# Optimization experiments

Measured on AMD Instinct MI355X. Metric: run time of the kernel, lower is better.

The kernel has to match this reference:

```python
import jax, jax.numpy as jnp
import numpy as np

EMBED_DIM = 512
NUM_HEADS = 8
HEAD_DIM = EMBED_DIM // NUM_HEADS


def setup_inputs() -> dict:
    key = jax.random.key(0)
    k1, k2, k3, k4, k5, k6 = jax.random.split(key, 6)
    B, S, D = 2, 4096, EMBED_DIM
    scale = 1.0 / np.sqrt(D)
    return {
        "inputs": jax.random.normal(k1, (B, S, D), dtype=jnp.float32),
        "Wq": jax.random.normal(k2, (D, D), dtype=jnp.float32) * scale,
        "Wk": jax.random.normal(k3, (D, D), dtype=jnp.float32) * scale,
        "Wv": jax.random.normal(k4, (D, D), dtype=jnp.float32) * scale,
        "Wc": jax.random.normal(k5, (D, D), dtype=jnp.float32) * scale,
        "bc": jax.random.normal(k6, (D,), dtype=jnp.float32) * 0.01,
    }


def reference(inputs, Wq, Wk, Wv, Wc, bc):
    B, S, D = inputs.shape
    H, Hd = NUM_HEADS, HEAD_DIM

    def split_heads(x):
        # [B,S,D] -> [B,H,S,Hd]
        return x.reshape(B, S, H, Hd).transpose(0, 2, 1, 3)

    # nn.Linear applies x @ W.T
    q = split_heads(inputs @ Wq.T).astype(jnp.float32)
    k = split_heads(inputs @ Wk.T).astype(jnp.float32)
    v = split_heads(inputs @ Wv.T).astype(jnp.float32)

    scores = jnp.einsum("bhqd,bhkd->bhqk", q, k) / np.sqrt(Hd).astype(jnp.float32)
    weights = jax.nn.softmax(scores, axis=-1)
    attended = jnp.einsum("bhqk,bhkd->bhqd", weights, v).astype(inputs.dtype)
    attended = attended.transpose(0, 2, 1, 3).reshape(B, S, D)
    return attended @ Wc.T + bc
```

## Files before the change

### kernel.cpp

```cpp
#include <hip/hip_runtime.h>
#include <cstdint>
#include <cstddef>

typedef _Float16 half_t;
typedef half_t h8 __attribute__((ext_vector_type(8)));
typedef half_t h4 __attribute__((ext_vector_type(4)));
typedef float f4 __attribute__((ext_vector_type(4)));
typedef float f16v __attribute__((ext_vector_type(16)));
typedef unsigned int u32;

static constexpr int S_LEN  = 4096;
static constexpr int DMODEL = 512;
static constexpr int NH     = 8;
static constexpr int HD     = 64;
static constexpr int BATCH  = 2;
static constexpr int MTOK   = BATCH * S_LEN;

#define QSCALE 0.18033688011112043f

__device__ __forceinline__ void g2lds16(const void* g, void* l) {
    __builtin_amdgcn_global_load_lds(
        (const __attribute__((address_space(1))) u32*)(uintptr_t)g,
        (__attribute__((address_space(3))) u32*)(u32)(uintptr_t)l,
        16, 0, 0);
}

__device__ __forceinline__ f4 mfma16(h8 a, h8 b, f4 c) {
    return __builtin_amdgcn_mfma_f32_16x16x32_f16(a, b, c, 0, 0, 0);
}

__device__ __forceinline__ f16v mfma32(h8 a, h8 b, f16v c) {
    return __builtin_amdgcn_mfma_f32_32x32x16_f16(a, b, c, 0, 0, 0);
}

__device__ __forceinline__ u32 pkrtz(float a, float b) {
#if __has_builtin(__builtin_amdgcn_cvt_pkrtz)
    auto r = __builtin_amdgcn_cvt_pkrtz(a, b);
    return __builtin_bit_cast(u32, r);
#else
    union { half_t h[2]; u32 u; } x;
    x.h[0] = (half_t)a; x.h[1] = (half_t)b;
    return x.u;
#endif
}

__device__ __forceinline__ void plswap(u32 a, u32 b, u32& lo, u32& hi_, int hi) {
#if __has_builtin(__builtin_amdgcn_permlane32_swap)
    auto r = __builtin_amdgcn_permlane32_swap(a, b, false, false);
    lo = (u32)r[0]; hi_ = (u32)r[1];
#else
    u32 ta = __shfl_xor(a, 32);
    u32 tb = __shfl_xor(b, 32);
    lo  = hi ? tb : a;
    hi_ = hi ? b  : ta;
#endif
}

__global__ void cvt_all(const float* __restrict__ X,
                        const float* __restrict__ w0, const float* __restrict__ w1,
                        const float* __restrict__ w2, const float* __restrict__ w3,
                        half_t* __restrict__ Xh,
                        half_t* __restrict__ o0, half_t* __restrict__ o1,
                        half_t* __restrict__ o2, half_t* __restrict__ o3) {
    int bx = blockIdx.x;
    const float* in;
    half_t* out;
    float s = 1.0f;
    int i;
    if (bx < 2048) {
        in = X; out = Xh;
        i = (bx * 256 + threadIdx.x) * 8;
    } else {
        int y = (bx - 2048) >> 7;
        in  = (y==0) ? w0 : (y==1) ? w1 : (y==2) ? w2 : w3;
        out = (y==0) ? o0 : (y==1) ? o1 : (y==2) ? o2 : o3;
        if (y == 0) s = QSCALE;
        i = (((bx - 2048) & 127) * 256 + threadIdx.x) * 8;
    }
    const float4* p = (const float4*)(in + i);
    float4 a = p[0], b = p[1];
    h8 h;
    h[0]=(half_t)(a.x*s); h[1]=(half_t)(a.y*s); h[2]=(half_t)(a.z*s); h[3]=(half_t)(a.w*s);
    h[4]=(half_t)(b.x*s); h[5]=(half_t)(b.y*s); h[6]=(half_t)(b.z*s); h[7]=(half_t)(b.w*s);
    *(h8*)(out + i) = h;
}

__device__ __forceinline__ void gemm_core4(const half_t* __restrict__ A,
                                           const half_t* __restrict__ B,
                                           int m0, int n0, int Kdim,
                                           half_t* As, half_t* Bs,
                                           f4 (&acc)[4][4]) {
    const int tid  = threadIdx.x;
    const int lane = tid & 63;
    const int w    = tid >> 6;
    const int quad = lane >> 4;
    const int low  = lane & 15;
    const int wr   = (w >> 1) * 64;
    const int wc   = (w & 1) * 64;

    f4 zero = {0.f, 0.f, 0.f, 0.f};
    #pragma unroll
    for (int i = 0; i < 4; ++i)
        #pragma unroll
        for (int j = 0; j < 4; ++j) acc[i][j] = zero;

    auto stage = [&](int kk, int p) {
        #pragma unroll
        for (int it = 0; it < 2; ++it) {
            int c = tid + 256 * it;
            int row = c >> 2, cs = c & 3;
            int gc = cs ^ ((row >> 1) & 3);
            g2lds16(A + (size_t)(m0 + row) * Kdim + kk + gc * 8, As + p * 4096 + c * 8);
        }
        #pragma unroll
        for (int it = 0; it < 2; ++it) {
            int c = tid + 256 * it;
            int row = c >> 2, cs = c & 3;
            int gc = cs ^ ((row >> 1) & 3);
            g2lds16(B + (size_t)(n0 + row) * Kdim + kk + gc * 8, Bs + p * 4096 + c * 8);
        }
    };

    stage(0, 0);
    const int T = Kdim / 32;
    for (int t = 0; t < T; ++t) {
        __syncthreads();
        if (t + 1 < T) stage((t + 1) * 32, (t + 1) & 1);

        const half_t* Ac = As + (t & 1) * 4096;
        const half_t* Bc = Bs + (t & 1) * 4096;
        h8 af[4], bf[4];
        #pragma unroll
        for (int i = 0; i < 4; ++i) {
            int r = wr + i * 16 + low;
            af[i] = *(const h8*)(Ac + r * 32 + (quad ^ ((r >> 1) & 3)) * 8);
        }
        #pragma unroll
        for (int j = 0; j < 4; ++j) {
            int r = wc + j * 16 + low;
            bf[j] = *(const h8*)(Bc + r * 32 + (quad ^ ((r >> 1) & 3)) * 8);
        }
        #pragma unroll
        for (int i = 0; i < 4; ++i)
            #pragma unroll
            for (int j = 0; j < 4; ++j)
                acc[i][j] = mfma16(af[i], bf[j], acc[i][j]);
    }
}

__global__ __launch_bounds__(256, 3) void gemm_proj(
    const half_t* __restrict__ X,
    const half_t* __restrict__ Wq, const half_t* __restrict__ Wk, const half_t* __restrict__ Wv,
    half_t* __restrict__ Q, half_t* __restrict__ K, half_t* __restrict__ Vt) {
    __shared__ half_t SM[16384];
    const int z  = blockIdx.z;
    const int bx = blockIdx.x;

    const half_t *A, *B;
    int m0, n0;
    if (z < 2) {
        A = X; B = (z == 0) ? Wq : Wk;
        m0 = (bx >> 2) * 128; n0 = (bx & 3) * 128;
    } else {
        A = Wv; B = X;
        m0 = (bx & 3) * 128; n0 = (bx >> 2) * 128;
    }
    f4 acc[4][4];
    gemm_core4(A, B, m0, n0, DMODEL, SM, SM + 8192, acc);

    const int tid  = threadIdx.x;
    const int lane = tid & 63;
    const int w    = tid >> 6;
    const int quad = lane >> 4, low = lane & 15;
    const int wr = (w >> 1) * 64, wc = (w & 1) * 64;

    __syncthreads();
    #pragma unroll
    for (int i = 0; i < 4; ++i) {
        #pragma unroll
        for (int j = 0; j < 4; ++j) {
            int coln = wc + j * 16 + low;
            #pragma unroll
            for (int r = 0; r < 4; ++r) {
                int row  = wr + i * 16 + quad * 4 + r;
                int sblk = (coln >> 3) ^ (((row >> 2) & 3) << 1);
                SM[row * 128 + sblk * 8 + (coln & 7)] = (half_t)acc[i][j][r];
            }
        }
    }
    __syncthreads();

    if (z < 2) {
        half_t* O = (z == 0) ? Q : K;
        #pragma unroll
        for (int it = 0; it < 8; ++it) {
            int c = tid + 256 * it;
            int row = c >> 4, blk = c & 15;
            h8 v = *(const h8*)(SM + row * 128 + (blk ^ (((row >> 2) & 3) << 1)) * 8);
            int m = m0 + row, n = n0 + blk * 8;
            int h = n >> 6, d = n & 63;
            int b = m >> 12, s = m & 4095;
            *(h8*)(O + (((size_t)(b * NH + h) << 12) + s) * 64 + d) = v;
        }
    } else {
        #pragma unroll
        for (int it = 0; it < 8; ++it) {
            int c = tid + 256 * it;
            int row = c >> 4, blk = c & 15;
            h8 v = *(const h8*)(SM + row * 128 + (blk ^ (((row >> 2) & 3) << 1)) * 8);
            int dg = m0 + row, tok = n0 + blk * 8;
            int b = tok >> 12, s = tok & 4095;
            *(h8*)(Vt + (((size_t)(b * NH + (dg >> 6))) << 18) + ((size_t)(dg & 63) << 12) + s) = v;
        }
    }
}

__global__ __launch_bounds__(256, 3) void gemm_out(
    const half_t* __restrict__ A, const half_t* __restrict__ W,
    const float* __restrict__ bias, float* __restrict__ out) {
    __shared__ half_t As[2 * 128 * 32];
    __shared__ half_t Bs[2 * 128 * 32];
    const int bx = blockIdx.x;
    const int m0 = (bx >> 2) * 128;
    const int n0 = (bx & 3) * 128;
    f4 acc[4][4];
    gemm_core4(A, W, m0, n0, DMODEL, As, Bs, acc);

    const int lane = threadIdx.x & 63;
    const int w    = threadIdx.x >> 6;
    const int quad = lane >> 4, low = lane & 15;
    const int wr = (w >> 1) * 64, wc = (w & 1) * 64;

    #pragma unroll
    for (int i = 0; i < 4; ++i) {
        int mb = m0 + wr + i * 16 + quad * 4;
        #pragma unroll
        for (int j = 0; j < 4; ++j) {
            int n = n0 + wc + j * 16 + low;
            float bv = bias[n];
            #pragma unroll
            for (int r = 0; r < 4; ++r)
                out[(size_t)(mb + r) * DMODEL + n] = acc[i][j][r] + bv;
        }
    }
}

__global__ __launch_bounds__(256, 2) void flash_attn(
    const half_t* __restrict__ Q,
    const half_t* __restrict__ K,
    const half_t* __restrict__ V,
    half_t* __restrict__ Oa) {
    __shared__ half_t Ks[2][128 * 64];
    __shared__ half_t Vs[2][64 * 128];

    const int tid  = threadIdx.x;
    const int lane = tid & 63;
    const int w    = tid >> 6;
    const int l31  = lane & 31;
    const int hi   = lane >> 5;
    const int bh   = blockIdx.y;
    const int q0   = blockIdx.x * 128 + w * 32;

    const half_t* Qb = Q + ((size_t)bh << 18);
    const half_t* Kb = K + ((size_t)bh << 18);
    const half_t* Vb = V + ((size_t)bh << 18);

    h8 qf[4];
    #pragma unroll
    for (int ks = 0; ks < 4; ++ks)
        qf[ks] = *(const h8*)(Qb + (size_t)(q0 + l31) * 64 + ks * 16 + hi * 8);

    f16v zz;
    #pragma unroll
    for (int r = 0; r < 16; ++r) zz[r] = 0.f;

    f16v Oacc[2];
    Oacc[0] = zz; Oacc[1] = zz;
    f4 rs = {0.f, 0.f, 0.f, 0.f};

    auto stage = [&](int k0, int p) {
        #pragma unroll
        for (int it = 0; it < 4; ++it) {
            int c = tid + 256 * it;
            int key = k0 + (c >> 8) * 32 + l31;
            int col = ((c >> 6) & 3) * 16 + hi * 8;
            g2lds16(Kb + (size_t)key * 64 + col, &Ks[p][c * 8]);
        }
        #pragma unroll
        for (int it = 0; it < 4; ++it) {
            int c = tid + 256 * it;
            int d   = (c >> 9) * 32 + l31;
            int key = k0 + ((c >> 6) & 7) * 16 + hi * 8;
            g2lds16(Vb + (size_t)d * S_LEN + key, &Vs[p][c * 8]);
        }
    };

    stage(0, 0);

    for (int c = 0; c < S_LEN / 128; ++c) {
        __syncthreads();
        if (c + 1 < S_LEN / 128) stage((c + 1) * 128, (c + 1) & 1);

        const half_t* Kl = Ks[c & 1] + lane * 8;
        const half_t* Vl = Vs[c & 1] + lane * 8;

        f16v sc[4];
        #pragma unroll
        for (int nt = 0; nt < 4; ++nt) {
            #pragma unroll
            for (int ks = 0; ks < 4; ++ks) {
                h8 kf = *(const h8*)(Kl + nt * 2048 + ks * 512);
                sc[nt] = mfma32(kf, qf[ks], ks == 0 ? zz : sc[nt]);
            }
        }

        #pragma unroll
        for (int nt = 0; nt < 4; ++nt) {
            float p[16];
            #pragma unroll
            for (int r = 0; r < 16; ++r) {
                p[r] = __builtin_amdgcn_exp2f(sc[nt][r]);
                rs[r & 3] += p[r];
            }
            u32 a0 = pkrtz(p[0],  p[1]);
            u32 a1 = pkrtz(p[2],  p[3]);
            u32 a2 = pkrtz(p[4],  p[5]);
            u32 a3 = pkrtz(p[6],  p[7]);
            u32 a4 = pkrtz(p[8],  p[9]);
            u32 a5 = pkrtz(p[10], p[11]);
            u32 a6 = pkrtz(p[12], p[13]);
            u32 a7 = pkrtz(p[14], p[15]);

            union H8U { u32 u[4]; h8 v; } b0, b1;
            plswap(a0, a2, b0.u[0], b0.u[2], hi);
            plswap(a1, a3, b0.u[1], b0.u[3], hi);
            plswap(a4, a6, b1.u[0], b1.u[2], hi);
            plswap(a5, a7, b1.u[1], b1.u[3], hi);

            #pragma unroll
            for (int dt = 0; dt < 2; ++dt) {
                h8 vf0 = *(const h8*)(Vl + dt * 4096 + (nt * 2 + 0) * 512);
                h8 vf1 = *(const h8*)(Vl + dt * 4096 + (nt * 2 + 1) * 512);
                Oacc[dt] = mfma32(vf0, b0.v, Oacc[dt]);
                Oacc[dt] = mfma32(vf1, b1.v, Oacc[dt]);
            }
        }
    }

    float lsum = (rs[0] + rs[1]) + (rs[2] + rs[3]);
    lsum += __shfl_xor(lsum, 32);
    float inv = 1.0f / lsum;

    const int b = bh >> 3, h = bh & 7;
    half_t* Ob = Oa + ((size_t)(b * S_LEN + q0 + l31)) * DMODEL + h * 64;
    #pragma unroll
    for (int dt = 0; dt < 2; ++dt)
        #pragma unroll
        for (int rg = 0; rg < 4; ++rg) {
            h4 o;
            #pragma unroll
            for (int e = 0; e < 4; ++e) o[e] = (half_t)(Oacc[dt][rg * 4 + e] * inv);
            *(h4*)(Ob + dt * 32 + rg * 8 + hi * 4) = o;
        }
}

extern "C" void kernel_launch(void* const* d_in, const int* in_sizes, int n_in,
                              void* d_out, int out_size, void* d_ws, size_t ws_size,
                              hipStream_t stream) {
    const float* X  = (const float*)d_in[0];
    const float* Wq = (const float*)d_in[1];
    const float* Wk = (const float*)d_in[2];
    const float* Wv = (const float*)d_in[3];
    const float* Wc = (const float*)d_in[4];
    const float* bc = (const float*)d_in[5];
    float* out = (float*)d_out;

    char* ws = (char*)d_ws;
    const size_t SZ_X = (size_t)MTOK * DMODEL * 2;
    const size_t SZ_W = (size_t)DMODEL * DMODEL * 2;
    half_t* Xh   = (half_t*)(ws);
    half_t* Wqh  = (half_t*)(ws + SZ_X);
    half_t* Wkh  = (half_t*)(ws + SZ_X + SZ_W);
    half_t* Wvh  = (half_t*)(ws + SZ_X + 2 * SZ_W);
    half_t* Wch  = (half_t*)(ws + SZ_X + 3 * SZ_W);
    half_t* Qh   = (half_t*)(ws + SZ_X + 4 * SZ_W);
    half_t* Kh   = (half_t*)(ws + 2 * SZ_X + 4 * SZ_W);
    half_t* Vt   = (half_t*)(ws + 3 * SZ_X + 4 * SZ_W);
    half_t* Att  = (half_t*)(ws + 4 * SZ_X + 4 * SZ_W);

    cvt_all<<<2048 + 512, 256, 0, stream>>>(X, Wq, Wk, Wv, Wc, Xh, Wqh, Wkh, Wvh, Wch);
    gemm_proj<<<dim3(256, 1, 3), 256, 0, stream>>>(Xh, Wqh, Wkh, Wvh, Qh, Kh, Vt);
    flash_attn<<<dim3(32, 16), 256, 0, stream>>>(Qh, Kh, Vt, Att);
    gemm_out<<<256, 256, 0, stream>>>(Att, Wch, bc, out);
}
```

Before: 191.2 us.

## Stage output GEMM epilogue through LDS and raise wave priority around attention MFMAs

The output projection epilogue now writes accumulators into a padded shared-memory tile in two halves, then reads them back as float4 rows and emits coalesced vector stores with the bias added. The previous per-element scattered float stores are replaced to cut global write transactions. Separately, the flash attention loop raises wave priority with s_setprio around the QK and PV MFMA blocks so matrix work is issued ahead of the exp/pack phases of other waves. The epilogue adds two extra barriers per half and enlarges the shared allocation, which may lower occupancy of the output GEMM.

```diff
diff --git a/kernel.cpp b/kernel.cpp
--- a/kernel.cpp
+++ b/kernel.cpp
@@ -218,29 +218,47 @@
 __global__ __launch_bounds__(256, 3) void gemm_out(
     const half_t* __restrict__ A, const half_t* __restrict__ W,
     const float* __restrict__ bias, float* __restrict__ out) {
-    __shared__ half_t As[2 * 128 * 32];
-    __shared__ half_t Bs[2 * 128 * 32];
+    __shared__ __align__(16) char SMX[36864];
+    half_t* As = (half_t*)SMX;
+    half_t* Bs = (half_t*)(SMX + 16384);
     const int bx = blockIdx.x;
     const int m0 = (bx >> 2) * 128;
     const int n0 = (bx & 3) * 128;
     f4 acc[4][4];
     gemm_core4(A, W, m0, n0, DMODEL, As, Bs, acc);
 
-    const int lane = threadIdx.x & 63;
-    const int w    = threadIdx.x >> 6;
+    const int tid  = threadIdx.x;
+    const int lane = tid & 63;
+    const int w    = tid >> 6;
     const int quad = lane >> 4, low = lane & 15;
-    const int wr = (w >> 1) * 64, wc = (w & 1) * 64;
-
-    #pragma unroll
-    for (int i = 0; i < 4; ++i) {
-        int mb = m0 + wr + i * 16 + quad * 4;
-        #pragma unroll
-        for (int j = 0; j < 4; ++j) {
-            int n = n0 + wc + j * 16 + low;
-            float bv = bias[n];
-            #pragma unroll
-            for (int r = 0; r < 4; ++r)
-                out[(size_t)(mb + r) * DMODEL + n] = acc[i][j][r] + bv;
+    const int wc = (w & 1) * 64;
+
+    float* C = (float*)SMX;
+    #pragma unroll
+    for (int p = 0; p < 2; ++p) {
+        __syncthreads();
+        if ((w >> 1) == p) {
+            #pragma unroll
+            for (int i = 0; i < 4; ++i)
+                #pragma unroll
+                for (int j = 0; j < 4; ++j) {
+                    int col = wc + j * 16 + low;
+                    #pragma unroll
+                    for (int r = 0; r < 4; ++r) {
+                        int lr = i * 16 + quad * 4 + r;
+                        C[lr * 132 + col] = acc[i][j][r];
+                    }
+                }
+        }
+        __syncthreads();
+        #pragma unroll
+        for (int it = 0; it < 8; ++it) {
+            int c = tid + 256 * it;
+            int lr = c >> 5, c4 = c & 31;
+            float4 v  = *(const float4*)(C + lr * 132 + c4 * 4);
+            float4 bv = *(const float4*)(bias + n0 + c4 * 4);
+            v.x += bv.x; v.y += bv.y; v.z += bv.z; v.w += bv.w;
+            *(float4*)(out + (size_t)(m0 + p * 64 + lr) * DMODEL + n0 + c4 * 4) = v;
         }
     }
 }
@@ -305,6 +323,7 @@
         const half_t* Vl = Vs[c & 1] + lane * 8;
 
         f16v sc[4];
+        __builtin_amdgcn_s_setprio(1);
         #pragma unroll
         for (int nt = 0; nt < 4; ++nt) {
             #pragma unroll
@@ -313,6 +332,7 @@
                 sc[nt] = mfma32(kf, qf[ks], ks == 0 ? zz : sc[nt]);
             }
         }
+        __builtin_amdgcn_s_setprio(0);
 
         #pragma unroll
         for (int nt = 0; nt < 4; ++nt) {
@@ -337,6 +357,7 @@
             plswap(a4, a6, b1.u[0], b1.u[2], hi);
             plswap(a5, a7, b1.u[1], b1.u[3], hi);
 
+            __builtin_amdgcn_s_setprio(1);
             #pragma unroll
             for (int dt = 0; dt < 2; ++dt) {
                 h8 vf0 = *(const h8*)(Vl + dt * 4096 + (nt * 2 + 0) * 512);
@@ -344,6 +365,7 @@
                 Oacc[dt] = mfma32(vf0, b0.v, Oacc[dt]);
                 Oacc[dt] = mfma32(vf1, b1.v, Oacc[dt]);
             }
+            __builtin_amdgcn_s_setprio(0);
         }
     }
 
```

New measurement: 196.9 us. +2.9%, slower.
